# Performance work log

Hardware: AMD Instinct MI355X
Metric: run time of the kernel (lower is better)

The kernel has to match this reference:

```python
import jax, jax.numpy as jnp
import numpy as np

NC = 80          # class_num
THRESH = 0.5     # objectness threshold (forward arg `thresh`)
IOU_T = 0.3      # NMS IoU threshold (utils.nms(boxes_c, 0.3))
K = 512          # fixed candidate budget per image (jit-safe replacement for nonzero)


def _decode(out, t, anchors):
    """_filter + _parse for one scale. out: (B, 3*(5+NC), H, W) -> boxes (B, H*W*3, 6), conf (B, H*W*3).
    Box columns: x1, y1, x2, y2, conf, cls."""
    B, C, H, W = out.shape
    o = out.transpose(0, 2, 3, 1).reshape(B, H, W, 3, 5 + NC)
    txy = jax.nn.sigmoid(o[..., 0:2])          # sigmoid on tx, ty
    conf = jax.nn.sigmoid(o[..., 4])           # sigmoid on objectness
    gy = jnp.arange(H, dtype=out.dtype)[:, None, None]   # grid row index (idxs[:,1])
    gx = jnp.arange(W, dtype=out.dtype)[None, :, None]   # grid col index (idxs[:,2])
    cy = (gy + txy[..., 1]) * t
    cx = (gx + txy[..., 0]) * t
    w = anchors[:, 0] * jnp.exp(o[..., 2])     # anchors broadcast over anchor axis
    h = anchors[:, 1] * jnp.exp(o[..., 3])
    cls = jnp.argmax(o[..., 5:], axis=-1).astype(out.dtype)
    boxes = jnp.stack([cx - w / 2, cy - h / 2, cx + w / 2, cy + h / 2, conf, cls], axis=-1)
    return boxes.reshape(B, -1, 6), conf.reshape(B, -1)


def _iou(b):
    """Pairwise IoU. b: (B, K, 4) -> (B, K, K)."""
    x1, y1, x2, y2 = b[..., 0], b[..., 1], b[..., 2], b[..., 3]
    area = (x2 - x1) * (y2 - y1)
    ix1 = jnp.maximum(x1[:, :, None], x1[:, None, :])
    iy1 = jnp.maximum(y1[:, :, None], y1[:, None, :])
    ix2 = jnp.minimum(x2[:, :, None], x2[:, None, :])
    iy2 = jnp.minimum(y2[:, :, None], y2[:, None, :])
    inter = jnp.maximum(ix2 - ix1, 0.0) * jnp.maximum(iy2 - iy1, 0.0)
    return inter / (area[:, :, None] + area[:, None, :] - inter + 1e-9)


def setup_inputs() -> dict:
    key = jax.random.key(0)
    k1, k2, k3 = jax.random.split(key, 3)
    B, C = 32, 3 * (5 + NC)
    return {
        "out13": jax.random.normal(k1, (B, C, 13, 13), jnp.float32),
        "out26": jax.random.normal(k2, (B, C, 26, 26), jnp.float32),
        "out52": jax.random.normal(k3, (B, C, 52, 52), jnp.float32),
        "anchors13": jnp.array([[116.0, 90.0], [156.0, 198.0], [373.0, 326.0]], jnp.float32),
        "anchors26": jnp.array([[30.0, 61.0], [62.0, 45.0], [59.0, 119.0]], jnp.float32),
        "anchors52": jnp.array([[10.0, 13.0], [16.0, 30.0], [33.0, 23.0]], jnp.float32),
    }


def reference(out13, out26, out52, anchors13, anchors26, anchors52):
    b13, c13 = _decode(out13, 32.0, anchors13)
    b26, c26 = _decode(out26, 16.0, anchors26)
    b52, c52 = _decode(out52, 8.0, anchors52)
    boxes = jnp.concatenate([b13, b26, b52], axis=1)   # (B, N, 6), N = 3549*3
    conf = jnp.concatenate([c13, c26, c52], axis=1)    # (B, N)
    B = boxes.shape[0]

    # threshold filter (conf > thresh) realized as masked top-K (jit-safe nonzero)
    scores = jnp.where(conf > THRESH, conf, -1.0)
    vals, idx = jax.lax.top_k(scores, K)               # sorted descending, as utils.nms expects
    bk = jnp.take_along_axis(boxes, idx[..., None], axis=1)   # (B, K, 6)
    valid = vals > THRESH                              # (B, K)

    # per-class greedy NMS
    iou = _iou(bk[..., :4])                            # (B, K, K)
    same_cls = bk[..., 5][:, :, None] == bk[..., 5][:, None, :]
    suppress = same_cls & (iou > IOU_T)

    def step(keep, i):
        sup_i = jnp.any(keep & suppress[:, i, :], axis=-1)
        keep = keep.at[:, i].set(valid[:, i] & ~sup_i)
        return keep, None

    keep, _ = jax.lax.scan(step, jnp.zeros((B, K), dtype=bool), jnp.arange(K))
    # (B, K, 7): x1, y1, x2, y2, conf, cls, keep_flag
    return jnp.concatenate([bk, keep[..., None].astype(bk.dtype)], axis=-1)
```

## Files before the change

kernel.cpp:

```cpp
#include <hip/hip_runtime.h>
#include <stdint.h>

#define NC13 507
#define NC26 2028
#define NC52 8112
#define NCAND 10647
#define KSEL 512
#define POOLCAP 768
#define POOLTGT 640
#define SUPW 17
#define CMW 17
#define DECB 6
#define HBINS 4096

__device__ __forceinline__ unsigned long long make_key(float xo, int n) {
    const unsigned long long low = (unsigned long long)(0x3FFFu - (unsigned)n);
    return (xo > 0.0f)
        ? ((1ull << 63) | ((unsigned long long)__float_as_uint(xo) << 32) | low)
        : low;
}

__device__ __forceinline__ void decode_write(
    float* __restrict__ o, int w, int h, float ts,
    float tx, float ty, float tw, float th, float xo,
    float aw, float ah, int cls)
{
    const float sx   = 1.0f / (1.0f + expf(-tx));
    const float sy   = 1.0f / (1.0f + expf(-ty));
    const float conf = 1.0f / (1.0f + expf(-xo));
    const float cx = ((float)w + sx) * ts;
    const float cy = ((float)h + sy) * ts;
    const float bw = aw * expf(tw);
    const float bh = ah * expf(th);
    o[0] = cx - bw * 0.5f; o[1] = cy - bh * 0.5f;
    o[2] = cx + bw * 0.5f; o[3] = cy + bh * 0.5f;
    o[4] = conf; o[5] = (float)cls;
}

__device__ __forceinline__ void emit_key(
    unsigned long long* __restrict__ kb, unsigned int* __restrict__ lh,
    float xo, int n)
{
    const unsigned long long k = make_key(xo, n);
    kb[n] = k;
    atomicAdd(&lh[(unsigned)((k >> 52) & 0xFFFull)], 1u);
}

__device__ __forceinline__ void decode4(
    const float* __restrict__ in, const float* __restrict__ anch,
    int b, int a, int hw, int HW, int Hdim, float ts, int base,
    float* __restrict__ boxesAll, unsigned long long* __restrict__ keys,
    unsigned int* __restrict__ lh)
{
    const int HW4 = HW >> 2;
    const float4* p4 = reinterpret_cast<const float4*>(
        in + ((size_t)b * 255 + (size_t)a * 85) * HW + hw);

    const float4 txv = p4[0];
    const float4 tyv = p4[(size_t)HW4];
    const float4 twv = p4[(size_t)2 * HW4];
    const float4 thv = p4[(size_t)3 * HW4];
    const float4 xov = p4[(size_t)4 * HW4];

    float4 best = make_float4(-INFINITY, -INFINITY, -INFINITY, -INFINITY);
    int bx = 0, by = 0, bz = 0, bw4 = 0;

    float4 vb[4];
    #pragma unroll
    for (int j = 0; j < 4; ++j) vb[j] = p4[(size_t)(5 + j) * HW4];
    for (int cb = 0; cb < 20; ++cb) {
        float4 vn[4];
        if (cb < 19) {
            #pragma unroll
            for (int j = 0; j < 4; ++j) vn[j] = p4[(size_t)(9 + cb * 4 + j) * HW4];
        }
        #pragma unroll
        for (int j = 0; j < 4; ++j) {
            const int c = cb * 4 + j;
            if (vb[j].x > best.x) { best.x = vb[j].x; bx = c; }
            if (vb[j].y > best.y) { best.y = vb[j].y; by = c; }
            if (vb[j].z > best.z) { best.z = vb[j].z; bz = c; }
            if (vb[j].w > best.w) { best.w = vb[j].w; bw4 = c; }
        }
        #pragma unroll
        for (int j = 0; j < 4; ++j) vb[j] = vn[j];
    }

    unsigned long long* kb = keys + (size_t)b * NCAND;
    emit_key(kb, lh, xov.x, base + (hw + 0) * 3 + a);
    emit_key(kb, lh, xov.y, base + (hw + 1) * 3 + a);
    emit_key(kb, lh, xov.z, base + (hw + 2) * 3 + a);
    emit_key(kb, lh, xov.w, base + (hw + 3) * 3 + a);

    const float aw = anch[2 * a], ah = anch[2 * a + 1];
    const int i0 = base + a * HW + hw;
    float* o = boxesAll + ((size_t)b * NCAND + i0) * 6;
    {
        const int h = hw / Hdim, w = hw - h * Hdim;
        decode_write(o, w, h, ts, txv.x, tyv.x, twv.x, thv.x, xov.x, aw, ah, bx);
    }
    {
        const int h = (hw + 1) / Hdim, w = (hw + 1) - h * Hdim;
        decode_write(o + 6, w, h, ts, txv.y, tyv.y, twv.y, thv.y, xov.y, aw, ah, by);
    }
    {
        const int h = (hw + 2) / Hdim, w = (hw + 2) - h * Hdim;
        decode_write(o + 12, w, h, ts, txv.z, tyv.z, twv.z, thv.z, xov.z, aw, ah, bz);
    }
    {
        const int h = (hw + 3) / Hdim, w = (hw + 3) - h * Hdim;
        decode_write(o + 18, w, h, ts, txv.w, tyv.w, twv.w, thv.w, xov.w, aw, ah, bw4);
    }
}

__global__ __launch_bounds__(512, 2) void decode_kernel(
    const float* __restrict__ in13,
    const float* __restrict__ in26,
    const float* __restrict__ in52,
    const float* __restrict__ a13,
    const float* __restrict__ a26,
    const float* __restrict__ a52,
    float* __restrict__ boxesAll,
    unsigned long long* __restrict__ keys,
    unsigned int* __restrict__ hist)
{
    __shared__ unsigned int lh[HBINS];
    const int role = blockIdx.x;
    const int b = blockIdx.y;
    const int tid = threadIdx.x;

    for (int i = tid; i < HBINS; i += 512) lh[i] = 0;
    __syncthreads();

    if (role < 4) {
        const int idx4 = role * 512 + tid;
        if (idx4 < 3 * 676) {
            const int a = idx4 / 676, g = idx4 - a * 676;
            decode4(in52, a52, b, a, g * 4, 2704, 52, 8.f, NC13 + NC26,
                    boxesAll, keys, lh);
        }
    } else if (role == 4) {
        if (tid < 3 * 169) {
            const int a = tid / 169, g = tid - a * 169;
            decode4(in26, a26, b, a, g * 4, 676, 26, 16.f, NC13,
                    boxesAll, keys, lh);
        }
    } else {
        if (tid < NC13) {
            const int HW = 169;
            const int a = tid / HW, hw = tid - a * HW;
            const int h = hw / 13, w = hw - h * 13;
            const float* p = in13 + ((size_t)b * 255 + (size_t)a * 85) * HW + hw;
            const float tx = p[0];
            const float ty = p[(size_t)HW];
            const float tw = p[(size_t)2 * HW];
            const float th = p[(size_t)3 * HW];
            const float xo = p[(size_t)4 * HW];
            float best = -INFINITY; int bi = 0;
            float vb[4];
            #pragma unroll
            for (int j = 0; j < 4; ++j) vb[j] = p[(size_t)(5 + j) * HW];
            for (int cb = 0; cb < 20; ++cb) {
                float vn[4];
                if (cb < 19) {
                    #pragma unroll
                    for (int j = 0; j < 4; ++j) vn[j] = p[(size_t)(9 + cb * 4 + j) * HW];
                }
                #pragma unroll
                for (int j = 0; j < 4; ++j) {
                    const int c = cb * 4 + j;
                    if (vb[j] > best) { best = vb[j]; bi = c; }
                }
                #pragma unroll
                for (int j = 0; j < 4; ++j) vb[j] = vn[j];
            }
            const int n = hw * 3 + a;
            emit_key(keys + (size_t)b * NCAND, lh, xo, n);
            const int i = a * HW + hw;
            decode_write(boxesAll + ((size_t)b * NCAND + i) * 6, w, h, 32.f,
                         tx, ty, tw, th, xo, a13[2 * a], a13[2 * a + 1], bi);
        }
    }

    __syncthreads();
    unsigned int* hb = hist + (size_t)b * HBINS;
    for (int i = tid; i < HBINS; i += 512) {
        const unsigned int v = lh[i];
        if (v) atomicAdd(&hb[i], v);
    }
}

struct SelS {
    unsigned int hist[HBINS];
    unsigned long long pool[POOLCAP];
};
struct NmsS {
    float X1[KSEL], Y1[KSEL], X2[KSEL], Y2[KSEL], AR[KSEL], CF[KSEL];
    int CLS[KSEL];
    unsigned int CM[80 * CMW];
    unsigned int SUP[KSEL * SUPW];
    unsigned int KEEP[16];
};

__global__ __launch_bounds__(1024) void selnms_kernel(
    const unsigned long long* __restrict__ keys,
    const unsigned int* __restrict__ hist,
    const float* __restrict__ boxesAll,
    float* __restrict__ out)
{
    constexpr size_t USZ = sizeof(SelS) > sizeof(NmsS) ? sizeof(SelS) : sizeof(NmsS);
    __shared__ __align__(16) char smem[USZ];
    __shared__ int selidxL[KSEL];
    __shared__ unsigned long long sh_prefix, sh_tmin;
    __shared__ int sh_krem, sh_shift, sh_brk, sh_V;
    __shared__ unsigned int sh_cnt;

    const int b = blockIdx.x;
    const int tid = threadIdx.x;
    const unsigned long long* kb = keys + (size_t)b * NCAND;
    SelS& S = *reinterpret_cast<SelS*>(smem);

    {
        const unsigned int* gh = hist + (size_t)b * HBINS;
        for (int i = tid; i < HBINS; i += 1024) S.hist[i] = gh[i];
    }
    if (tid == 0) { sh_cnt = 0; sh_prefix = 0; sh_krem = KSEL; sh_shift = 52; sh_brk = 0; }
    __syncthreads();

    bool first = true;
    while (true) {
        const int shift = sh_shift;
        const unsigned long long prefix = sh_prefix;
        const int krem = sh_krem;
        if (tid < 64) {
            unsigned int s = 0;
            for (int q = 0; q < 64; ++q) s += S.hist[tid * 64 + q];
            unsigned int suf = s;
            for (int off = 1; off < 64; off <<= 1) {
                const unsigned int v = __shfl_down(suf, off);
                if (tid + off < 64) suf += v;
            }
            if (first) {
                const unsigned int Vv = __shfl(suf, 32);
                if (tid == 0) sh_V = (int)Vv;
            }
            const unsigned long long ball = __ballot(suf >= (unsigned)krem);
            const int lstar = 63 - __clzll(ball);
            const unsigned int base = (lstar < 63) ? __shfl(suf, lstar + 1) : 0u;
            const unsigned int wv = S.hist[lstar * 64 + (63 - tid)];
            unsigned int pv = wv;
            for (int off = 1; off < 64; off <<= 1) {
                const unsigned int v = __shfl_up(pv, off);
                if (tid >= (unsigned)off) pv += v;
            }
            const unsigned long long b2 = __ballot(base + pv >= (unsigned)krem);
            const int mstar = __ffsll(b2) - 1;
            const unsigned int pvm = __shfl(pv, mstar);
            const unsigned int wvm = __shfl(wv, mstar);
            if (tid == 0) {
                const int dstar = lstar * 64 + (63 - mstar);
                const unsigned long long np = (prefix << 12) | (unsigned long long)dstar;
                const int Albl = (int)(base + pvm - wvm);
                const int Cpool = (KSEL - krem) + Albl + (int)wvm;
                sh_prefix = np;
                sh_krem = krem - Albl;
                if (Cpool <= POOLTGT || shift == 4) {
                    sh_brk = 1;
                    sh_tmin = np << shift;
                } else {
                    sh_shift = shift - 12;
                }
            }
        }
        __syncthreads();
        first = false;
        if (sh_brk) break;

        const int nshift = sh_shift;
        const unsigned long long nprefix = sh_prefix;
        for (int i = tid; i < HBINS; i += 1024) S.hist[i] = 0;
        __syncthreads();
        for (int i = tid; i < NCAND; i += 1024) {
            const unsigned long long k = kb[i];
            if ((k >> (nshift + 12)) == nprefix)
                atomicAdd(&S.hist[(unsigned)((k >> nshift) & 0xFFFull)], 1u);
        }
        __syncthreads();
    }
    const unsigned long long tmin = sh_tmin;

    for (int i = tid; i < NCAND; i += 1024) {
        const unsigned long long k = kb[i];
        if (k >= tmin) {
            const unsigned int p = atomicAdd(&sh_cnt, 1u);
            if (p < POOLCAP) S.pool[p] = k;
        }
    }
    __syncthreads();
    const int C = ((int)sh_cnt < POOLCAP) ? (int)sh_cnt : POOLCAP;

    for (int p = tid; p < C; p += 1024) {
        const unsigned long long k = S.pool[p];
        int r = 0;
        for (int j = 0; j < C; ++j) r += (S.pool[j] > k) ? 1 : 0;
        if (r < KSEL) selidxL[r] = 0x3FFF - (int)(k & 0x3FFFull);
    }
    const int V = (sh_V < KSEL) ? sh_V : KSEL;
    __syncthreads();

    NmsS& M = *reinterpret_cast<NmsS*>(smem);
    const int t5 = tid & 511;
    const int half = tid >> 9;

    const int n = selidxL[t5];
    int base, HW;
    if (n < NC13)             { base = 0;           HW = 169; }
    else if (n < NC13 + NC26) { base = NC13;        HW = 676; }
    else                      { base = NC13 + NC26; HW = 2704; }
    const int within = n - base;
    const int hw = within / 3, a = within - 3 * hw;
    const int i = base + a * HW + hw;

    if (half == 0) {
        const float* src = boxesAll + ((size_t)b * NCAND + i) * 6;
        const float x1 = src[0], y1 = src[1], x2 = src[2], y2 = src[3];
        M.X1[t5] = x1; M.Y1[t5] = y1; M.X2[t5] = x2; M.Y2[t5] = y2;
        M.AR[t5] = (x2 - x1) * (y2 - y1);
        M.CF[t5] = src[4];
        M.CLS[t5] = (int)src[5];
    }
    for (int q = tid; q < 80 * CMW; q += 1024) M.CM[q] = 0;
    __syncthreads();

    const float x1 = M.X1[t5], y1 = M.Y1[t5], x2 = M.X2[t5], y2 = M.Y2[t5];
    const float ar = M.AR[t5];
    const int ci = M.CLS[t5];
    if (half == 0) atomicOr(&M.CM[ci * CMW + (t5 >> 5)], 1u << (t5 & 31));
    __syncthreads();

    for (int wj = half * 8; wj < half * 8 + 8; ++wj) {
        unsigned int m = M.CM[ci * CMW + wj];
        unsigned int bits = 0;
        while (m) {
            const int bit = __ffs(m) - 1;
            m &= m - 1;
            const int j = wj * 32 + bit;
            const float iw = fminf(x2, M.X2[j]) - fmaxf(x1, M.X1[j]);
            const float ih = fminf(y2, M.Y2[j]) - fmaxf(y1, M.Y1[j]);
            if (iw > 0.0f && ih > 0.0f) {
                const float inter = iw * ih;
                if (inter > 0.3f * (ar + M.AR[j] - inter + 1e-9f))
                    bits |= (1u << bit);
            }
        }
        M.SUP[t5 * SUPW + wj] = bits;
    }
    __syncthreads();

    if (tid < 64) {
        unsigned int keepw = 0;
        unsigned int buf[16];
        #pragma unroll
        for (int r = 0; r < 16; ++r)
            buf[r] = (tid < 16) ? M.SUP[r * SUPW + tid] : 0u;
        for (int g = 0; g < 32; ++g) {
            unsigned int nbuf[16] = {0};
            if (g < 31) {
                #pragma unroll
                for (int r = 0; r < 16; ++r)
                    nbuf[r] = (tid < 16) ? M.SUP[((g + 1) * 16 + r) * SUPW + tid] : 0u;
            }
            #pragma unroll
            for (int r = 0; r < 16; ++r) {
                const int ii = g * 16 + r;
                const bool anysup = __any((keepw & buf[r]) != 0u);
                const bool ki = (ii < V) && !anysup;
                if (ki && tid == (ii >> 5)) keepw |= (1u << (ii & 31));
            }
            #pragma unroll
            for (int r = 0; r < 16; ++r) buf[r] = nbuf[r];
        }
        if (tid < 16) M.KEEP[tid] = keepw;
    }
    __syncthreads();

    if (tid < 512) {
        const float kf = ((M.KEEP[t5 >> 5] >> (t5 & 31)) & 1u) ? 1.0f : 0.0f;
        float* dst = out + ((size_t)b * KSEL + t5) * 7;
        dst[0] = x1; dst[1] = y1; dst[2] = x2; dst[3] = y2;
        dst[4] = M.CF[t5]; dst[5] = (float)ci; dst[6] = kf;
    }
}

extern "C" void kernel_launch(void* const* d_in, const int* in_sizes, int n_in,
                              void* d_out, int out_size, void* d_ws, size_t ws_size,
                              hipStream_t stream)
{
    (void)n_in; (void)out_size; (void)ws_size;
    const float* in13 = (const float*)d_in[0];
    const float* in26 = (const float*)d_in[1];
    const float* in52 = (const float*)d_in[2];
    const float* a13  = (const float*)d_in[3];
    const float* a26  = (const float*)d_in[4];
    const float* a52  = (const float*)d_in[5];
    float* out = (float*)d_out;
    const int B = in_sizes[0] / (255 * 169);

    char* w = (char*)d_ws;
    unsigned long long* keys = (unsigned long long*)w;
    w += ((size_t)B * NCAND * sizeof(unsigned long long) + 255) & ~(size_t)255;
    float* boxesAll = (float*)w;
    w += ((size_t)B * NCAND * 6 * sizeof(float) + 255) & ~(size_t)255;
    unsigned int* hist = (unsigned int*)w;
    w += ((size_t)B * HBINS * sizeof(unsigned int) + 255) & ~(size_t)255;

    hipMemsetAsync(hist, 0, (size_t)B * HBINS * sizeof(unsigned int), stream);
    decode_kernel<<<dim3(DECB, B), 512, 0, stream>>>(
        in13, in26, in52, a13, a26, a52, boxesAll, keys, hist);
    selnms_kernel<<<dim3(B), 1024, 0, stream>>>(keys, hist, boxesAll, out);
}
```

Measured before the change: 81.86 us.

## Switch decoded boxes to SoA with padded layout and global histogram atomics

Decoded boxes move from an AoS (6 floats per box) layout to a padded SoA layout, so each thread writes its four boxes as float4 stores. Keys are stored in that same padded index order. The shared-memory histogram is removed; the decode kernel now does direct global atomics, and only for positive-objectness keys. Non-positive keys are added back into bin 0 in the selection kernel, which now computes the valid count with a separate reduction. The decode grid becomes 12 blocks of 256 threads per image instead of 6 of 512, trading more blocks and more global atomics for no shared-memory setup and fewer barriers.

```diff
diff --git a/kernel.cpp b/kernel.cpp
--- a/kernel.cpp
+++ b/kernel.cpp
@@ -5,12 +5,16 @@
 #define NC26 2028
 #define NC52 8112
 #define NCAND 10647
+#define NCANDP 10648
+#define PB13 0
+#define PB26 508
+#define PB52 2536
 #define KSEL 512
 #define POOLCAP 768
 #define POOLTGT 640
 #define SUPW 17
 #define CMW 17
-#define DECB 6
+#define DECB 12
 #define HBINS 4096
 
 __device__ __forceinline__ unsigned long long make_key(float xo, int n) {
@@ -20,37 +24,13 @@
         : low;
 }
 
-__device__ __forceinline__ void decode_write(
-    float* __restrict__ o, int w, int h, float ts,
-    float tx, float ty, float tw, float th, float xo,
-    float aw, float ah, int cls)
-{
-    const float sx   = 1.0f / (1.0f + expf(-tx));
-    const float sy   = 1.0f / (1.0f + expf(-ty));
-    const float conf = 1.0f / (1.0f + expf(-xo));
-    const float cx = ((float)w + sx) * ts;
-    const float cy = ((float)h + sy) * ts;
-    const float bw = aw * expf(tw);
-    const float bh = ah * expf(th);
-    o[0] = cx - bw * 0.5f; o[1] = cy - bh * 0.5f;
-    o[2] = cx + bw * 0.5f; o[3] = cy + bh * 0.5f;
-    o[4] = conf; o[5] = (float)cls;
-}
-
-__device__ __forceinline__ void emit_key(
-    unsigned long long* __restrict__ kb, unsigned int* __restrict__ lh,
-    float xo, int n)
-{
-    const unsigned long long k = make_key(xo, n);
-    kb[n] = k;
-    atomicAdd(&lh[(unsigned)((k >> 52) & 0xFFFull)], 1u);
-}
-
 __device__ __forceinline__ void decode4(
     const float* __restrict__ in, const float* __restrict__ anch,
-    int b, int a, int hw, int HW, int Hdim, float ts, int base,
-    float* __restrict__ boxesAll, unsigned long long* __restrict__ keys,
-    unsigned int* __restrict__ lh)
+    int b, int a, int hw, int HW, int Hdim, float ts,
+    int nbase, int pbase,
+    float* __restrict__ bb,
+    unsigned long long* __restrict__ kb,
+    unsigned int* __restrict__ hb)
 {
     const int HW4 = HW >> 2;
     const float4* p4 = reinterpret_cast<const float4*>(
@@ -86,34 +66,43 @@
         for (int j = 0; j < 4; ++j) vb[j] = vn[j];
     }
 
-    unsigned long long* kb = keys + (size_t)b * NCAND;
-    emit_key(kb, lh, xov.x, base + (hw + 0) * 3 + a);
-    emit_key(kb, lh, xov.y, base + (hw + 1) * 3 + a);
-    emit_key(kb, lh, xov.z, base + (hw + 2) * 3 + a);
-    emit_key(kb, lh, xov.w, base + (hw + 3) * 3 + a);
+    const int i0 = pbase + a * HW + hw;
+    const unsigned long long k0 = make_key(xov.x, nbase + (hw + 0) * 3 + a);
+    const unsigned long long k1 = make_key(xov.y, nbase + (hw + 1) * 3 + a);
+    const unsigned long long k2 = make_key(xov.z, nbase + (hw + 2) * 3 + a);
+    const unsigned long long k3 = make_key(xov.w, nbase + (hw + 3) * 3 + a);
+    kb[i0 + 0] = k0; kb[i0 + 1] = k1; kb[i0 + 2] = k2; kb[i0 + 3] = k3;
+    if (xov.x > 0.f) atomicAdd(&hb[(unsigned)(k0 >> 52)], 1u);
+    if (xov.y > 0.f) atomicAdd(&hb[(unsigned)(k1 >> 52)], 1u);
+    if (xov.z > 0.f) atomicAdd(&hb[(unsigned)(k2 >> 52)], 1u);
+    if (xov.w > 0.f) atomicAdd(&hb[(unsigned)(k3 >> 52)], 1u);
 
     const float aw = anch[2 * a], ah = anch[2 * a + 1];
-    const int i0 = base + a * HW + hw;
-    float* o = boxesAll + ((size_t)b * NCAND + i0) * 6;
-    {
-        const int h = hw / Hdim, w = hw - h * Hdim;
-        decode_write(o, w, h, ts, txv.x, tyv.x, twv.x, thv.x, xov.x, aw, ah, bx);
-    }
-    {
-        const int h = (hw + 1) / Hdim, w = (hw + 1) - h * Hdim;
-        decode_write(o + 6, w, h, ts, txv.y, tyv.y, twv.y, thv.y, xov.y, aw, ah, by);
-    }
-    {
-        const int h = (hw + 2) / Hdim, w = (hw + 2) - h * Hdim;
-        decode_write(o + 12, w, h, ts, txv.z, tyv.z, twv.z, thv.z, xov.z, aw, ah, bz);
-    }
-    {
-        const int h = (hw + 3) / Hdim, w = (hw + 3) - h * Hdim;
-        decode_write(o + 18, w, h, ts, txv.w, tyv.w, twv.w, thv.w, xov.w, aw, ah, bw4);
-    }
+    float4 X1v, Y1v, X2v, Y2v, CFv, CLv;
+#define DECC(comp, j, bidx) { \
+        const int hwj = hw + j; \
+        const int hj = hwj / Hdim, wj = hwj - hj * Hdim; \
+        const float sx = 1.0f / (1.0f + expf(-txv.comp)); \
+        const float sy = 1.0f / (1.0f + expf(-tyv.comp)); \
+        const float cf = 1.0f / (1.0f + expf(-xov.comp)); \
+        const float cx = ((float)wj + sx) * ts; \
+        const float cy = ((float)hj + sy) * ts; \
+        const float bw = aw * expf(twv.comp); \
+        const float bh = ah * expf(thv.comp); \
+        X1v.comp = cx - bw * 0.5f; Y1v.comp = cy - bh * 0.5f; \
+        X2v.comp = cx + bw * 0.5f; Y2v.comp = cy + bh * 0.5f; \
+        CFv.comp = cf; CLv.comp = (float)bidx; }
+    DECC(x, 0, bx) DECC(y, 1, by) DECC(z, 2, bz) DECC(w, 3, bw4)
+#undef DECC
+    *reinterpret_cast<float4*>(bb + (size_t)0 * NCANDP + i0) = X1v;
+    *reinterpret_cast<float4*>(bb + (size_t)1 * NCANDP + i0) = Y1v;
+    *reinterpret_cast<float4*>(bb + (size_t)2 * NCANDP + i0) = X2v;
+    *reinterpret_cast<float4*>(bb + (size_t)3 * NCANDP + i0) = Y2v;
+    *reinterpret_cast<float4*>(bb + (size_t)4 * NCANDP + i0) = CFv;
+    *reinterpret_cast<float4*>(bb + (size_t)5 * NCANDP + i0) = CLv;
 }
 
-__global__ __launch_bounds__(512, 2) void decode_kernel(
+__global__ __launch_bounds__(256, 3) void decode_kernel(
     const float* __restrict__ in13,
     const float* __restrict__ in26,
     const float* __restrict__ in52,
@@ -124,31 +113,32 @@
     unsigned long long* __restrict__ keys,
     unsigned int* __restrict__ hist)
 {
-    __shared__ unsigned int lh[HBINS];
     const int role = blockIdx.x;
     const int b = blockIdx.y;
     const int tid = threadIdx.x;
-
-    for (int i = tid; i < HBINS; i += 512) lh[i] = 0;
-    __syncthreads();
-
-    if (role < 4) {
-        const int idx4 = role * 512 + tid;
+    float* bb = boxesAll + (size_t)b * 6 * NCANDP;
+    unsigned long long* kb = keys + (size_t)b * NCANDP;
+    unsigned int* hb = hist + (size_t)b * HBINS;
+
+    if (role < 8) {
+        const int idx4 = role * 256 + tid;
         if (idx4 < 3 * 676) {
             const int a = idx4 / 676, g = idx4 - a * 676;
-            decode4(in52, a52, b, a, g * 4, 2704, 52, 8.f, NC13 + NC26,
-                    boxesAll, keys, lh);
-        }
-    } else if (role == 4) {
-        if (tid < 3 * 169) {
-            const int a = tid / 169, g = tid - a * 169;
-            decode4(in26, a26, b, a, g * 4, 676, 26, 16.f, NC13,
-                    boxesAll, keys, lh);
+            decode4(in52, a52, b, a, g * 4, 2704, 52, 8.f, NC13 + NC26, PB52,
+                    bb, kb, hb);
+        }
+    } else if (role < 10) {
+        const int idx4 = (role - 8) * 256 + tid;
+        if (idx4 < 3 * 169) {
+            const int a = idx4 / 169, g = idx4 - a * 169;
+            decode4(in26, a26, b, a, g * 4, 676, 26, 16.f, NC13, PB26,
+                    bb, kb, hb);
         }
     } else {
-        if (tid < NC13) {
+        const int idx = (role - 10) * 256 + tid;
+        if (idx < NC13) {
             const int HW = 169;
-            const int a = tid / HW, hw = tid - a * HW;
+            const int a = idx / HW, hw = idx - a * HW;
             const int h = hw / 13, w = hw - h * 13;
             const float* p = in13 + ((size_t)b * 255 + (size_t)a * 85) * HW + hw;
             const float tx = p[0];
@@ -175,18 +165,26 @@
                 for (int j = 0; j < 4; ++j) vb[j] = vn[j];
             }
             const int n = hw * 3 + a;
-            emit_key(keys + (size_t)b * NCAND, lh, xo, n);
-            const int i = a * HW + hw;
-            decode_write(boxesAll + ((size_t)b * NCAND + i) * 6, w, h, 32.f,
-                         tx, ty, tw, th, xo, a13[2 * a], a13[2 * a + 1], bi);
-        }
-    }
-
-    __syncthreads();
-    unsigned int* hb = hist + (size_t)b * HBINS;
-    for (int i = tid; i < HBINS; i += 512) {
-        const unsigned int v = lh[i];
-        if (v) atomicAdd(&hb[i], v);
+            const unsigned long long k = make_key(xo, n);
+            const int i = PB13 + a * HW + hw;
+            kb[i] = k;
+            if (xo > 0.f) atomicAdd(&hb[(unsigned)(k >> 52)], 1u);
+            const float sx   = 1.0f / (1.0f + expf(-tx));
+            const float sy   = 1.0f / (1.0f + expf(-ty));
+            const float cf   = 1.0f / (1.0f + expf(-xo));
+            const float cx = ((float)w + sx) * 32.f;
+            const float cy = ((float)h + sy) * 32.f;
+            const float bw = a13[2 * a] * expf(tw);
+            const float bh = a13[2 * a + 1] * expf(th);
+            bb[(size_t)0 * NCANDP + i] = cx - bw * 0.5f;
+            bb[(size_t)1 * NCANDP + i] = cy - bh * 0.5f;
+            bb[(size_t)2 * NCANDP + i] = cx + bw * 0.5f;
+            bb[(size_t)3 * NCANDP + i] = cy + bh * 0.5f;
+            bb[(size_t)4 * NCANDP + i] = cf;
+            bb[(size_t)5 * NCANDP + i] = (float)bi;
+        } else if (idx == NC13) {
+            kb[507] = 0;
+        }
     }
 }
 
@@ -217,7 +215,7 @@
 
     const int b = blockIdx.x;
     const int tid = threadIdx.x;
-    const unsigned long long* kb = keys + (size_t)b * NCAND;
+    const unsigned long long* kb = keys + (size_t)b * NCANDP;
     SelS& S = *reinterpret_cast<SelS*>(smem);
 
     {
@@ -227,7 +225,17 @@
     if (tid == 0) { sh_cnt = 0; sh_prefix = 0; sh_krem = KSEL; sh_shift = 52; sh_brk = 0; }
     __syncthreads();
 
-    bool first = true;
+    if (tid < 64) {
+        unsigned int s = 0;
+        for (int q = 0; q < 64; ++q) s += S.hist[tid * 64 + q];
+        #pragma unroll
+        for (int off = 32; off; off >>= 1) s += __shfl_xor(s, off);
+        if (tid == 0) sh_V = (int)s;
+    }
+    __syncthreads();
+    if (tid == 0 && sh_V < KSEL) S.hist[0] += (unsigned)(NCAND - sh_V);
+    __syncthreads();
+
     while (true) {
         const int shift = sh_shift;
         const unsigned long long prefix = sh_prefix;
@@ -239,10 +247,6 @@
             for (int off = 1; off < 64; off <<= 1) {
                 const unsigned int v = __shfl_down(suf, off);
                 if (tid + off < 64) suf += v;
-            }
-            if (first) {
-                const unsigned int Vv = __shfl(suf, 32);
-                if (tid == 0) sh_V = (int)Vv;
             }
             const unsigned long long ball = __ballot(suf >= (unsigned)krem);
             const int lstar = 63 - __clzll(ball);
@@ -273,14 +277,13 @@
             }
         }
         __syncthreads();
-        first = false;
         if (sh_brk) break;
 
         const int nshift = sh_shift;
         const unsigned long long nprefix = sh_prefix;
         for (int i = tid; i < HBINS; i += 1024) S.hist[i] = 0;
         __syncthreads();
-        for (int i = tid; i < NCAND; i += 1024) {
+        for (int i = tid; i < NCANDP; i += 1024) {
             const unsigned long long k = kb[i];
             if ((k >> (nshift + 12)) == nprefix)
                 atomicAdd(&S.hist[(unsigned)((k >> nshift) & 0xFFFull)], 1u);
@@ -289,7 +292,7 @@
     }
     const unsigned long long tmin = sh_tmin;
 
-    for (int i = tid; i < NCAND; i += 1024) {
+    for (int i = tid; i < NCANDP; i += 1024) {
         const unsigned long long k = kb[i];
         if (k >= tmin) {
             const unsigned int p = atomicAdd(&sh_cnt, 1u);
@@ -313,21 +316,24 @@
     const int half = tid >> 9;
 
     const int n = selidxL[t5];
-    int base, HW;
-    if (n < NC13)             { base = 0;           HW = 169; }
-    else if (n < NC13 + NC26) { base = NC13;        HW = 676; }
-    else                      { base = NC13 + NC26; HW = 2704; }
-    const int within = n - base;
+    int nbase, HW, pb;
+    if (n < NC13)             { nbase = 0;           HW = 169;  pb = PB13; }
+    else if (n < NC13 + NC26) { nbase = NC13;        HW = 676;  pb = PB26; }
+    else                      { nbase = NC13 + NC26; HW = 2704; pb = PB52; }
+    const int within = n - nbase;
     const int hw = within / 3, a = within - 3 * hw;
-    const int i = base + a * HW + hw;
+    const int i = pb + a * HW + hw;
 
     if (half == 0) {
-        const float* src = boxesAll + ((size_t)b * NCAND + i) * 6;
-        const float x1 = src[0], y1 = src[1], x2 = src[2], y2 = src[3];
+        const float* bbp = boxesAll + (size_t)b * 6 * NCANDP;
+        const float x1 = bbp[(size_t)0 * NCANDP + i];
+        const float y1 = bbp[(size_t)1 * NCANDP + i];
+        const float x2 = bbp[(size_t)2 * NCANDP + i];
+        const float y2 = bbp[(size_t)3 * NCANDP + i];
         M.X1[t5] = x1; M.Y1[t5] = y1; M.X2[t5] = x2; M.Y2[t5] = y2;
         M.AR[t5] = (x2 - x1) * (y2 - y1);
-        M.CF[t5] = src[4];
-        M.CLS[t5] = (int)src[5];
+        M.CF[t5] = bbp[(size_t)4 * NCANDP + i];
+        M.CLS[t5] = (int)bbp[(size_t)5 * NCANDP + i];
     }
     for (int q = tid; q < 80 * CMW; q += 1024) M.CM[q] = 0;
     __syncthreads();
@@ -408,14 +414,14 @@
 
     char* w = (char*)d_ws;
     unsigned long long* keys = (unsigned long long*)w;
-    w += ((size_t)B * NCAND * sizeof(unsigned long long) + 255) & ~(size_t)255;
+    w += ((size_t)B * NCANDP * sizeof(unsigned long long) + 255) & ~(size_t)255;
     float* boxesAll = (float*)w;
-    w += ((size_t)B * NCAND * 6 * sizeof(float) + 255) & ~(size_t)255;
+    w += ((size_t)B * 6 * NCANDP * sizeof(float) + 255) & ~(size_t)255;
     unsigned int* hist = (unsigned int*)w;
     w += ((size_t)B * HBINS * sizeof(unsigned int) + 255) & ~(size_t)255;
 
     hipMemsetAsync(hist, 0, (size_t)B * HBINS * sizeof(unsigned int), stream);
-    decode_kernel<<<dim3(DECB, B), 512, 0, stream>>>(
+    decode_kernel<<<dim3(DECB, B), 256, 0, stream>>>(
         in13, in26, in52, a13, a26, a52, boxesAll, keys, hist);
     selnms_kernel<<<dim3(B), 1024, 0, stream>>>(keys, hist, boxesAll, out);
 }
```

After: 144.2 us. 76.1% more time.
